# Optimization experiments

Hardware: AMD Instinct MI355X
Metric: run time of the kernel (lower is better)

The kernel has to match this reference:

```python
import math
import jax, jax.numpy as jnp
import numpy as np

B, N, L, D, H = 1, 64, 512, 768, 12
DK = D // H


def setup_inputs() -> dict:
    rng = jax.random.key(0)
    ks = jax.random.split(rng, 8)
    s = 0.02  # weight init scale
    return {
        "query": jax.random.normal(ks[0], (B, N, L, D), jnp.float32),
        "key": jax.random.normal(ks[1], (B, N, L, D), jnp.float32),
        "value": jax.random.normal(ks[2], (B, N, L, D), jnp.float32),
        "Wq": jax.random.normal(ks[3], (D, D), jnp.float32) * s,
        "bq": jnp.zeros((D,), jnp.float32),
        "Wk": jax.random.normal(ks[4], (D, D), jnp.float32) * s,
        "bk": jnp.zeros((D,), jnp.float32),
        "Wv": jax.random.normal(ks[5], (D, D), jnp.float32) * s,
        "bv": jnp.zeros((D,), jnp.float32),
        "Wo": jax.random.normal(ks[6], (D, D), jnp.float32) * s,
        "bo": jnp.zeros((D,), jnp.float32),
    }


def reference(query, key, value, Wq, bq, Wk, bk, Wv, bv, Wo, bo):
    b, n, l, d = query.shape
    h, dk = H, DK
    # combined scaling: 1/sqrt(d_k) * 1/sqrt(N)
    scale = 1.0 / (math.sqrt(dk) * math.sqrt(n))
    # nn.Linear: y = x @ W.T + b  (W is [out, in])
    q = (jnp.einsum('bnld,ed->bnle', query, Wq) + bq).reshape(b, n, l, h, dk) * scale
    k = (jnp.einsum('bnld,ed->bnle', key, Wk) + bk).reshape(b, n, l, h, dk)
    v = (jnp.einsum('bnld,ed->bnle', value, Wv) + bv).reshape(b, n, l, h, dk)
    # tied attention: scores summed over the N (sequence-copy) axis BEFORE softmax
    att = jnp.einsum('bnihk,bnjhk->bhij', q, k)  # [B,H,L,L]
    att = jax.nn.softmax(att, axis=-1)  # dropout is identity in eval
    # single attention map broadcast across all N value tensors
    out = jnp.einsum('bhij,bnjhk->bnihk', att, v).reshape(b, n, l, d)
    return jnp.einsum('bnld,ed->bnle', out, Wo) + bo
```

## Files before the change

kernel.cpp:

```cpp
#include <hip/hip_runtime.h>


typedef __bf16 bf16x8 __attribute__((ext_vector_type(8)));
typedef float f32x4 __attribute__((ext_vector_type(4)));

__device__ __forceinline__ unsigned short f2bf(float f) {
  unsigned u = __float_as_uint(f);
  u += 0x7fffu + ((u >> 16) & 1u);
  return (unsigned short)(u >> 16);
}

__device__ __forceinline__ void gll16(const unsigned short* g, unsigned short* l) {
  __builtin_amdgcn_global_load_lds(
      (const __attribute__((address_space(1))) unsigned int*)g,
      (__attribute__((address_space(3))) unsigned int*)l, 16, 0, 0);
}

template <bool C, typename T1, typename T2> struct Cond { using type = T1; };
template <typename T1, typename T2> struct Cond<false, T1, T2> { using type = T2; };

enum { MODE_QCAT = 0, MODE_VT = 1, MODE_ATT = 2, MODE_OUTWS = 3, MODE_OUT_BIAS = 4 };

constexpr int BM = 128, BN = 128, BK = 32;

template <int MODE, bool F32S, bool SWZ, int KS>
__global__ __launch_bounds__(256, 2) void gemm_bt(
    const void* __restrict__ Av, const void* __restrict__ Bv,
    const float* __restrict__ bias, void* __restrict__ Cv,
    int K, int lda, int ldb, long long a_bs, long long b_bs,
    float alpha, int ntn) {
  using T = typename Cond<F32S, float, unsigned short>::type;
  constexpr int LP = F32S ? 40 : 32;

  __shared__ unsigned short As[BM * LP];
  __shared__ unsigned short Bs[BN * LP];

  const int tid = threadIdx.x;
  const int wave = tid >> 6;
  const int lane = tid & 63;
  const int wm = wave >> 1, wn = wave & 1;

  int tm, tn;
  if constexpr (SWZ) {
    const int bid = blockIdx.x;
    const int xcd = bid & 7;
    const int k = bid >> 3;
    tn = k % ntn;
    tm = (k / ntn) * 8 + xcd;
  } else {
    tn = blockIdx.x;
    tm = blockIdx.y;
  }
  int batch = blockIdx.z, ks = 0;
  if constexpr (KS > 1) { ks = batch % KS; batch /= KS; }

  const long long m0 = (long long)tm * BM;
  const long long n0 = (long long)tn * BN;

  const T* Ab = (const T*)Av + (long long)batch * a_bs + (long long)ks * K;
  const T* Bb = (const T*)Bv + (long long)batch * b_bs + (long long)ks * K;

  f32x4 acc[4][4] = {};

  const int l15 = lane & 15;
  const int kq = (lane >> 4) * 8;

  for (int k0 = 0; k0 < K; k0 += BK) {
    if constexpr (F32S) {
      const int row = tid >> 3;
      const int c4 = (tid & 7) * 4;
#pragma unroll
      for (int rr = 0; rr < 4; ++rr) {
        const int r = row + rr * 32;
        const float4 av = *(const float4*)((const float*)Ab + (m0 + r) * (long long)lda + k0 + c4);
        const float4 bv = *(const float4*)((const float*)Bb + (n0 + r) * (long long)ldb + k0 + c4);
        ushort4 ap{f2bf(av.x), f2bf(av.y), f2bf(av.z), f2bf(av.w)};
        ushort4 bp{f2bf(bv.x), f2bf(bv.y), f2bf(bv.z), f2bf(bv.w)};
        *(ushort4*)&As[r * LP + c4] = ap;
        *(ushort4*)&Bs[r * LP + c4] = bp;
      }
    } else {
      const int r_in = lane >> 2;
      const int c8 = (lane & 3) * 8;
#pragma unroll
      for (int t = 0; t < 2; ++t) {
        const int rb = t * 64 + wave * 16;
        gll16((const unsigned short*)Ab + (m0 + rb + r_in) * (long long)lda + k0 + c8,
              &As[rb * LP]);
        gll16((const unsigned short*)Bb + (n0 + rb + r_in) * (long long)ldb + k0 + c8,
              &Bs[rb * LP]);
      }
    }
    __syncthreads();

    bf16x8 af[4], bfr[4];
#pragma unroll
    for (int t = 0; t < 4; ++t)
      af[t] = *(const bf16x8*)&As[(wm * 64 + t * 16 + l15) * LP + kq];
#pragma unroll
    for (int u = 0; u < 4; ++u)
      bfr[u] = *(const bf16x8*)&Bs[(wn * 64 + u * 16 + l15) * LP + kq];
#pragma unroll
    for (int t = 0; t < 4; ++t)
#pragma unroll
      for (int u = 0; u < 4; ++u)
        acc[t][u] = __builtin_amdgcn_mfma_f32_16x16x32_bf16(af[t], bfr[u], acc[t][u], 0, 0, 0);
    __syncthreads();
  }

#pragma unroll
  for (int t = 0; t < 4; ++t) {
#pragma unroll
    for (int u = 0; u < 4; ++u) {
      const long long col = n0 + wn * 64 + u * 16 + l15;
#pragma unroll
      for (int r = 0; r < 4; ++r) {
        const long long row = m0 + wm * 64 + t * 16 + (lane >> 4) * 4 + r;
        float v = acc[t][u][r];
        if constexpr (MODE == MODE_QCAT) {
          v = (v + bias[col]) * alpha;
          const long long h = col >> 6, kk = col & 63, n = row >> 9, i = row & 511;
          ((unsigned short*)Cv)[((h * 512 + i) << 12) + (n << 6) + kk] = f2bf(v);
        } else if constexpr (MODE == MODE_VT) {
          v = v + bias[col];
          const long long h = col >> 6, kk = col & 63, n = row >> 9, j = row & 511;
          ((unsigned short*)Cv)[(((h << 12) + (n << 6) + kk) << 9) + j] = f2bf(v);
        } else if constexpr (MODE == MODE_ATT) {
          float* p = &((float*)Cv)[((long long)batch << 18) + (row << 9) + col];
          if constexpr (KS > 1) atomicAdd(p, v); else *p = v;
        } else if constexpr (MODE == MODE_OUTWS) {
          const long long n = col >> 6, kk = col & 63;
          ((unsigned short*)Cv)[(n * 512 + row) * 768 + (long long)batch * 64 + kk] = f2bf(v);
        } else {
          ((float*)Cv)[row * 768 + col] = v + bias[col];
        }
      }
    }
  }
}

__global__ __launch_bounds__(256) void softmax_rows(const float* __restrict__ att,
                                                    unsigned short* __restrict__ outb) {
  const long long rowbase = (long long)blockIdx.x << 9;
  const int tid = threadIdx.x;
  float a = att[rowbase + tid];
  float b = att[rowbase + tid + 256];

  float m = fmaxf(a, b);
#pragma unroll
  for (int off = 32; off; off >>= 1) m = fmaxf(m, __shfl_down(m, off));
  __shared__ float redm[4];
  if ((tid & 63) == 0) redm[tid >> 6] = m;
  __syncthreads();
  m = fmaxf(fmaxf(redm[0], redm[1]), fmaxf(redm[2], redm[3]));

  const float e0 = __expf(a - m), e1 = __expf(b - m);
  float s = e0 + e1;
#pragma unroll
  for (int off = 32; off; off >>= 1) s += __shfl_down(s, off);
  __shared__ float reds[4];
  if ((tid & 63) == 0) reds[tid >> 6] = s;
  __syncthreads();
  s = reds[0] + reds[1] + reds[2] + reds[3];

  const float inv = 1.0f / s;
  outb[rowbase + tid] = f2bf(e0 * inv);
  outb[rowbase + tid + 256] = f2bf(e1 * inv);
}

__global__ __launch_bounds__(256) void cvt_bf16(const float* __restrict__ in,
                                                unsigned short* __restrict__ out) {
  const long long i = ((long long)blockIdx.x * 256 + threadIdx.x) * 8;
  const float4 a = *(const float4*)(in + i);
  const float4 b = *(const float4*)(in + i + 4);
  uint4 p;
  p.x = (unsigned)f2bf(a.x) | ((unsigned)f2bf(a.y) << 16);
  p.y = (unsigned)f2bf(a.z) | ((unsigned)f2bf(a.w) << 16);
  p.z = (unsigned)f2bf(b.x) | ((unsigned)f2bf(b.y) << 16);
  p.w = (unsigned)f2bf(b.z) | ((unsigned)f2bf(b.w) << 16);
  *(uint4*)(out + i) = p;
}

__global__ __launch_bounds__(256) void cvt_w4(
    const float* __restrict__ s0, const float* __restrict__ s1,
    const float* __restrict__ s2, const float* __restrict__ s3,
    unsigned short* __restrict__ d0, unsigned short* __restrict__ d1,
    unsigned short* __restrict__ d2, unsigned short* __restrict__ d3) {
  const float* s;
  unsigned short* d;
  switch (blockIdx.y) {
    case 0: s = s0; d = d0; break;
    case 1: s = s1; d = d1; break;
    case 2: s = s2; d = d2; break;
    default: s = s3; d = d3; break;
  }
  const long long i = ((long long)blockIdx.x * 256 + threadIdx.x) * 8;
  const float4 a = *(const float4*)(s + i);
  const float4 b = *(const float4*)(s + i + 4);
  uint4 p;
  p.x = (unsigned)f2bf(a.x) | ((unsigned)f2bf(a.y) << 16);
  p.y = (unsigned)f2bf(a.z) | ((unsigned)f2bf(a.w) << 16);
  p.z = (unsigned)f2bf(b.x) | ((unsigned)f2bf(b.y) << 16);
  p.w = (unsigned)f2bf(b.z) | ((unsigned)f2bf(b.w) << 16);
  *(uint4*)(d + i) = p;
}

extern "C" void kernel_launch(void* const* d_in, const int* in_sizes, int n_in,
                              void* d_out, int out_size, void* d_ws, size_t ws_size,
                              hipStream_t stream) {
  const float* query = (const float*)d_in[0];
  const float* key   = (const float*)d_in[1];
  const float* value = (const float*)d_in[2];
  const float* Wq = (const float*)d_in[3];
  const float* bq = (const float*)d_in[4];
  const float* Wk = (const float*)d_in[5];
  const float* bk = (const float*)d_in[6];
  const float* Wv = (const float*)d_in[7];
  const float* bv = (const float*)d_in[8];
  const float* Wo = (const float*)d_in[9];
  const float* bo = (const float*)d_in[10];
  float* out = (float*)d_out;

  char* ws = (char*)d_ws;
  unsigned short* q_ws  = (unsigned short*)(ws);
  unsigned short* k_ws  = (unsigned short*)(ws + 50331648);
  unsigned short* vt_ws = (unsigned short*)(ws + 100663296);
  float*          att   = (float*)(ws + 150994944);
  unsigned short* wo_b  = (unsigned short*)(ws + 163577856);
  unsigned short* wq_b  = (unsigned short*)(ws + 150994944);
  unsigned short* wk_b  = (unsigned short*)(ws + 150994944 + 1179648);
  unsigned short* wv_b  = (unsigned short*)(ws + 150994944 + 2359296);
  unsigned short* att_b = k_ws;
  unsigned short* out_ws = q_ws;
  unsigned short* xb = (unsigned short*)d_out;

  const dim3 blk(256);

  cvt_w4<<<dim3(288, 4), blk, 0, stream>>>(Wo, Wq, Wk, Wv, wo_b, wq_b, wk_b, wv_b);

  cvt_bf16<<<12288, blk, 0, stream>>>(query, xb);
  gemm_bt<MODE_QCAT, false, true, 1><<<dim3(1536, 1, 1), blk, 0, stream>>>(
      xb, wq_b, bq, q_ws, 768, 768, 768, 0, 0, 0.015625f, 6);
  cvt_bf16<<<12288, blk, 0, stream>>>(key, xb);
  gemm_bt<MODE_QCAT, false, true, 1><<<dim3(1536, 1, 1), blk, 0, stream>>>(
      xb, wk_b, bk, k_ws, 768, 768, 768, 0, 0, 1.0f, 6);
  cvt_bf16<<<12288, blk, 0, stream>>>(value, xb);
  gemm_bt<MODE_VT, false, true, 1><<<dim3(1536, 1, 1), blk, 0, stream>>>(
      xb, wv_b, bv, vt_ws, 768, 768, 768, 0, 0, 1.0f, 6);

  hipMemsetAsync(att, 0, 12582912, stream);
  gemm_bt<MODE_ATT, false, false, 4><<<dim3(4, 4, 48), blk, 0, stream>>>(
      q_ws, k_ws, nullptr, att, 1024, 4096, 4096, 2097152LL, 2097152LL, 1.0f, 4);

  softmax_rows<<<6144, blk, 0, stream>>>(att, att_b);

  gemm_bt<MODE_OUTWS, false, false, 1><<<dim3(32, 4, 12), blk, 0, stream>>>(
      att_b, vt_ws, nullptr, out_ws, 512, 512, 512, 262144LL, 2097152LL, 1.0f, 32);

  gemm_bt<MODE_OUT_BIAS, false, true, 1><<<dim3(1536, 1, 1), blk, 0, stream>>>(
      out_ws, wo_b, bo, out, 768, 768, 768, 0, 0, 1.0f, 6);
}
```

Measured before the change: 693.9 us.

## Batch Q/K projection into one launch and add XCD-aware swizzle for attention GEMMs

Converts query and key to bf16 in a single two-slice kernel into two halves of the output buffer, then runs Q and K projections as one batched GEMM launch selecting bias/scale per batch. The attention-score and attention-value GEMMs switch from 3D grids to a 1D grid remapped so blocks sharing operands land on the same XCD, aiming at better L2 reuse. The unused fp32-staging path is removed. Costs are extra index arithmetic and a larger staging footprint in the output buffer.

```diff
diff --git a/kernel.cpp b/kernel.cpp
--- a/kernel.cpp
+++ b/kernel.cpp
@@ -16,21 +16,18 @@
       (__attribute__((address_space(3))) unsigned int*)l, 16, 0, 0);
 }
 
-template <bool C, typename T1, typename T2> struct Cond { using type = T1; };
-template <typename T1, typename T2> struct Cond<false, T1, T2> { using type = T2; };
-
 enum { MODE_QCAT = 0, MODE_VT = 1, MODE_ATT = 2, MODE_OUTWS = 3, MODE_OUT_BIAS = 4 };
 
 constexpr int BM = 128, BN = 128, BK = 32;
 
-template <int MODE, bool F32S, bool SWZ, int KS>
+template <int MODE, bool SWZ, int KS>
 __global__ __launch_bounds__(256, 2) void gemm_bt(
     const void* __restrict__ Av, const void* __restrict__ Bv,
     const float* __restrict__ bias, void* __restrict__ Cv,
     int K, int lda, int ldb, long long a_bs, long long b_bs,
-    float alpha, int ntn) {
-  using T = typename Cond<F32S, float, unsigned short>::type;
-  constexpr int LP = F32S ? 40 : 32;
+    float alpha, int ntn,
+    const float* __restrict__ bias2, float alpha2, long long c_bs) {
+  constexpr int LP = 32;
 
   __shared__ unsigned short As[BM * LP];
   __shared__ unsigned short Bs[BN * LP];
@@ -40,56 +37,60 @@
   const int lane = tid & 63;
   const int wm = wave >> 1, wn = wave & 1;
 
-  int tm, tn;
-  if constexpr (SWZ) {
+  int tm, tn, batch = 0, ks = 0;
+  if constexpr (SWZ && MODE == MODE_ATT) {
     const int bid = blockIdx.x;
-    const int xcd = bid & 7;
-    const int k = bid >> 3;
-    tn = k % ntn;
-    tm = (k / ntn) * 8 + xcd;
+    const int xcd = bid & 7, j = bid >> 3;
+    const int z = (j >> 4) * 8 + xcd;
+    const int tile = j & 15;
+    tn = tile & 3;
+    tm = tile >> 2;
+    ks = z % KS;
+    batch = z / KS;
+  } else if constexpr (SWZ && MODE == MODE_OUTWS) {
+    const int bid = blockIdx.x;
+    const int xcd = bid & 7, j = bid >> 3;
+    const int g = (j >> 6) * 8 + xcd;
+    const int idx = j & 63;
+    batch = g >> 1;
+    tm = idx >> 4;
+    tn = (g & 1) * 16 + (idx & 15);
   } else {
-    tn = blockIdx.x;
-    tm = blockIdx.y;
-  }
-  int batch = blockIdx.z, ks = 0;
-  if constexpr (KS > 1) { ks = batch % KS; batch /= KS; }
+    if constexpr (SWZ) {
+      const int bid = blockIdx.x;
+      const int xcd = bid & 7;
+      const int k = bid >> 3;
+      tn = k % ntn;
+      tm = (k / ntn) * 8 + xcd;
+    } else {
+      tn = blockIdx.x;
+      tm = blockIdx.y;
+    }
+    batch = blockIdx.z;
+    if constexpr (KS > 1) { ks = batch % KS; batch /= KS; }
+  }
 
   const long long m0 = (long long)tm * BM;
   const long long n0 = (long long)tn * BN;
 
-  const T* Ab = (const T*)Av + (long long)batch * a_bs + (long long)ks * K;
-  const T* Bb = (const T*)Bv + (long long)batch * b_bs + (long long)ks * K;
+  const unsigned short* Ab = (const unsigned short*)Av + (long long)batch * a_bs + (long long)ks * K;
+  const unsigned short* Bb = (const unsigned short*)Bv + (long long)batch * b_bs + (long long)ks * K;
 
   f32x4 acc[4][4] = {};
 
   const int l15 = lane & 15;
   const int kq = (lane >> 4) * 8;
+  const int r_in = lane >> 2;
+  const int c8 = (lane & 3) * 8;
 
   for (int k0 = 0; k0 < K; k0 += BK) {
-    if constexpr (F32S) {
-      const int row = tid >> 3;
-      const int c4 = (tid & 7) * 4;
-#pragma unroll
-      for (int rr = 0; rr < 4; ++rr) {
-        const int r = row + rr * 32;
-        const float4 av = *(const float4*)((const float*)Ab + (m0 + r) * (long long)lda + k0 + c4);
-        const float4 bv = *(const float4*)((const float*)Bb + (n0 + r) * (long long)ldb + k0 + c4);
-        ushort4 ap{f2bf(av.x), f2bf(av.y), f2bf(av.z), f2bf(av.w)};
-        ushort4 bp{f2bf(bv.x), f2bf(bv.y), f2bf(bv.z), f2bf(bv.w)};
-        *(ushort4*)&As[r * LP + c4] = ap;
-        *(ushort4*)&Bs[r * LP + c4] = bp;
-      }
-    } else {
-      const int r_in = lane >> 2;
-      const int c8 = (lane & 3) * 8;
-#pragma unroll
-      for (int t = 0; t < 2; ++t) {
-        const int rb = t * 64 + wave * 16;
-        gll16((const unsigned short*)Ab + (m0 + rb + r_in) * (long long)lda + k0 + c8,
-              &As[rb * LP]);
-        gll16((const unsigned short*)Bb + (n0 + rb + r_in) * (long long)ldb + k0 + c8,
-              &Bs[rb * LP]);
-      }
+#pragma unroll
+    for (int t = 0; t < 2; ++t) {
+      const int rb = t * 64 + wave * 16;
+      gll16((const unsigned short*)Ab + (m0 + rb + r_in) * (long long)lda + k0 + c8,
+            &As[rb * LP]);
+      gll16((const unsigned short*)Bb + (n0 + rb + r_in) * (long long)ldb + k0 + c8,
+            &Bs[rb * LP]);
     }
     __syncthreads();
 
@@ -118,9 +119,11 @@
         const long long row = m0 + wm * 64 + t * 16 + (lane >> 4) * 4 + r;
         float v = acc[t][u][r];
         if constexpr (MODE == MODE_QCAT) {
-          v = (v + bias[col]) * alpha;
+          const float* bb = batch ? bias2 : bias;
+          const float aa = batch ? alpha2 : alpha;
+          v = (v + bb[col]) * aa;
           const long long h = col >> 6, kk = col & 63, n = row >> 9, i = row & 511;
-          ((unsigned short*)Cv)[((h * 512 + i) << 12) + (n << 6) + kk] = f2bf(v);
+          ((unsigned short*)Cv + batch * c_bs)[((h * 512 + i) << 12) + (n << 6) + kk] = f2bf(v);
         } else if constexpr (MODE == MODE_VT) {
           v = v + bias[col];
           const long long h = col >> 6, kk = col & 63, n = row >> 9, j = row & 511;
@@ -181,6 +184,22 @@
   *(uint4*)(out + i) = p;
 }
 
+__global__ __launch_bounds__(256) void cvt_qk(
+    const float* __restrict__ s0, const float* __restrict__ s1,
+    unsigned short* __restrict__ d0, unsigned short* __restrict__ d1) {
+  const float* s = blockIdx.y ? s1 : s0;
+  unsigned short* d = blockIdx.y ? d1 : d0;
+  const long long i = ((long long)blockIdx.x * 256 + threadIdx.x) * 8;
+  const float4 a = *(const float4*)(s + i);
+  const float4 b = *(const float4*)(s + i + 4);
+  uint4 p;
+  p.x = (unsigned)f2bf(a.x) | ((unsigned)f2bf(a.y) << 16);
+  p.y = (unsigned)f2bf(a.z) | ((unsigned)f2bf(a.w) << 16);
+  p.z = (unsigned)f2bf(b.x) | ((unsigned)f2bf(b.y) << 16);
+  p.w = (unsigned)f2bf(b.z) | ((unsigned)f2bf(b.w) << 16);
+  *(uint4*)(d + i) = p;
+}
+
 __global__ __launch_bounds__(256) void cvt_w4(
     const float* __restrict__ s0, const float* __restrict__ s1,
     const float* __restrict__ s2, const float* __restrict__ s3,
@@ -232,31 +251,34 @@
   unsigned short* wv_b  = (unsigned short*)(ws + 150994944 + 2359296);
   unsigned short* att_b = k_ws;
   unsigned short* out_ws = q_ws;
-  unsigned short* xb = (unsigned short*)d_out;
+  unsigned short* xb0 = (unsigned short*)d_out;
+  unsigned short* xb1 = (unsigned short*)d_out + 25165824;
 
   const dim3 blk(256);
 
   cvt_w4<<<dim3(288, 4), blk, 0, stream>>>(Wo, Wq, Wk, Wv, wo_b, wq_b, wk_b, wv_b);
 
-  cvt_bf16<<<12288, blk, 0, stream>>>(query, xb);
-  gemm_bt<MODE_QCAT, false, true, 1><<<dim3(1536, 1, 1), blk, 0, stream>>>(
-      xb, wq_b, bq, q_ws, 768, 768, 768, 0, 0, 0.015625f, 6);
-  cvt_bf16<<<12288, blk, 0, stream>>>(key, xb);
-  gemm_bt<MODE_QCAT, false, true, 1><<<dim3(1536, 1, 1), blk, 0, stream>>>(
-      xb, wk_b, bk, k_ws, 768, 768, 768, 0, 0, 1.0f, 6);
-  cvt_bf16<<<12288, blk, 0, stream>>>(value, xb);
-  gemm_bt<MODE_VT, false, true, 1><<<dim3(1536, 1, 1), blk, 0, stream>>>(
-      xb, wv_b, bv, vt_ws, 768, 768, 768, 0, 0, 1.0f, 6);
+  cvt_qk<<<dim3(12288, 2), blk, 0, stream>>>(query, key, xb0, xb1);
+
+  gemm_bt<MODE_QCAT, true, 1><<<dim3(1536, 1, 2), blk, 0, stream>>>(
+      xb0, wq_b, bq, q_ws, 768, 768, 768, 25165824LL, 589824LL, 0.015625f, 6,
+      bk, 1.0f, 25165824LL);
+
+  cvt_bf16<<<12288, blk, 0, stream>>>(value, xb0);
+  gemm_bt<MODE_VT, true, 1><<<dim3(1536, 1, 1), blk, 0, stream>>>(
+      xb0, wv_b, bv, vt_ws, 768, 768, 768, 0, 0, 1.0f, 6, nullptr, 0.0f, 0);
 
   hipMemsetAsync(att, 0, 12582912, stream);
-  gemm_bt<MODE_ATT, false, false, 4><<<dim3(4, 4, 48), blk, 0, stream>>>(
-      q_ws, k_ws, nullptr, att, 1024, 4096, 4096, 2097152LL, 2097152LL, 1.0f, 4);
+  gemm_bt<MODE_ATT, true, 4><<<dim3(768, 1, 1), blk, 0, stream>>>(
+      q_ws, k_ws, nullptr, att, 1024, 4096, 4096, 2097152LL, 2097152LL, 1.0f, 0,
+      nullptr, 0.0f, 0);
 
   softmax_rows<<<6144, blk, 0, stream>>>(att, att_b);
 
-  gemm_bt<MODE_OUTWS, false, false, 1><<<dim3(32, 4, 12), blk, 0, stream>>>(
-      att_b, vt_ws, nullptr, out_ws, 512, 512, 512, 262144LL, 2097152LL, 1.0f, 32);
-
-  gemm_bt<MODE_OUT_BIAS, false, true, 1><<<dim3(1536, 1, 1), blk, 0, stream>>>(
-      out_ws, wo_b, bo, out, 768, 768, 768, 0, 0, 1.0f, 6);
-}
+  gemm_bt<MODE_OUTWS, true, 1><<<dim3(1536, 1, 1), blk, 0, stream>>>(
+      att_b, vt_ws, nullptr, out_ws, 512, 512, 512, 262144LL, 2097152LL, 1.0f, 0,
+      nullptr, 0.0f, 0);
+
+  gemm_bt<MODE_OUT_BIAS, true, 1><<<dim3(1536, 1, 1), blk, 0, stream>>>(
+      out_ws, wo_b, bo, out, 768, 768, 768, 0, 0, 1.0f, 6, nullptr, 0.0f, 0);
+}
```

New measurement: 668.2 us. -3.7%, faster.
